# Performance work log

Hardware: AMD Instinct MI355X
Metric: run time of the kernel (lower is better)

## Reference

```python
import jax, jax.numpy as jnp
import numpy as np

BN_EPS = 1e-5


def setup_inputs() -> dict:
    key = jax.random.key(0)
    ks = jax.random.split(key, 6)
    B, N, M, C1, C2 = 8, 8192, 2048, 128, 256
    in_ch = C1 + C2  # 384
    return {
        "xyz1": jax.random.uniform(ks[0], (B, N, 3), dtype=jnp.float32),
        "xyz2": jax.random.uniform(ks[1], (B, M, 3), dtype=jnp.float32),
        "features1": jax.random.normal(ks[2], (B, C1, N), dtype=jnp.float32),
        "features2": jax.random.normal(ks[3], (B, C2, M), dtype=jnp.float32),
        # Conv1d(kernel_size=1, bias=False) weights, squeezed to [out, in]
        "conv_w0": jax.random.normal(ks[4], (256, in_ch), dtype=jnp.float32) * 0.05,
        "gamma0": jnp.ones((256,), dtype=jnp.float32),
        "beta0": jnp.zeros((256,), dtype=jnp.float32),
        "conv_w1": jax.random.normal(ks[5], (256, 256), dtype=jnp.float32) * 0.05,
        "gamma1": jnp.ones((256,), dtype=jnp.float32),
        "beta1": jnp.zeros((256,), dtype=jnp.float32),
    }


def _conv_bn_relu(x, w, gamma, beta):
    # 1x1 Conv1d (no bias) == per-point channel matmul: [B,Cin,N] -> [B,Cout,N]
    x = jnp.einsum("oc,bcn->bon", w, x)
    # BatchNorm1d in training mode: batch stats over (B, N), biased variance
    mu = jnp.mean(x, axis=(0, 2), keepdims=True)
    var = jnp.var(x, axis=(0, 2), keepdims=True)
    x = (x - mu) * jax.lax.rsqrt(var + BN_EPS)
    x = x * gamma[None, :, None] + beta[None, :, None]
    return jax.nn.relu(x)


def reference(xyz1, xyz2, features1, features2,
              conv_w0, gamma0, beta0, conv_w1, gamma1, beta1):
    # squared pairwise distances [B, N, M] (broadcast diff reduced over coord dim)
    diff = xyz1[:, :, None, :] - xyz2[:, None, :, :]  # [B,N,M,3]
    dists = jnp.sum(diff * diff, axis=-1)             # [B,N,M]
    idx = jnp.argmin(dists, axis=-1)                  # [B,N] nearest downsampled point

    # per-batch gather: features2[b, :, idx[b]] -> [B, C2, N]
    interp = jax.vmap(lambda f, i: f[:, i])(features2, idx)

    x = jnp.concatenate([features1, interp], axis=1)  # [B, C1+C2, N]
    x = _conv_bn_relu(x, conv_w0, gamma0, beta0)
    x = _conv_bn_relu(x, conv_w1, gamma1, beta1)
    return x
```

## Files before the change

kernel.cpp:

```cpp
#include <hip/hip_runtime.h>
#include <stdint.h>

typedef unsigned short u16;
typedef unsigned int u32;
typedef __attribute__((ext_vector_type(8))) short short8;
typedef __attribute__((ext_vector_type(4))) float floatx4;

__device__ __forceinline__ u16 f2b(float f) {
  union { float f; u32 u; } c; c.f = f;
  u32 u = c.u;
  u += 0x7fffu + ((u >> 16) & 1u);
  return (u16)(u >> 16);
}
__device__ __forceinline__ float b2f(u16 h) {
  union { u32 u; float f; } c; c.u = ((u32)h) << 16;
  return c.f;
}

__device__ __forceinline__ void glds16(const void* g, void* l) {
  __builtin_amdgcn_global_load_lds((__attribute__((address_space(1))) void*)g,
                                   (__attribute__((address_space(3))) void*)l, 16, 0, 0);
}

__global__ void prep_all_k(const float* __restrict__ xyz1, const float* __restrict__ xyz2,
                           float2* __restrict__ cand,
                           const float* __restrict__ f1, u16* __restrict__ f1t,
                           const float* __restrict__ f2, u16* __restrict__ f2t,
                           const float* __restrict__ w0, u16* __restrict__ w0b,
                           const float* __restrict__ w1, u16* __restrict__ w1b,
                           float* __restrict__ sums) {
  __shared__ __align__(16) char smem[9216];
  int blk = blockIdx.x, t = threadIdx.x;
  if (blk < 512) {
    float4* s2 = (float4*)smem;
    int nq = blk & 7, mq = (blk >> 3) & 7, b = blk >> 6;
    const float* x2 = xyz2 + ((size_t)b * 2048 + mq * 256) * 3;
    s2[t] = make_float4(x2[t * 3], x2[t * 3 + 1], x2[t * 3 + 2], 0.f);
    __syncthreads();
    int n0 = nq * 1024 + t;
    float px[4], py[4], pz[4];
#pragma unroll
    for (int q = 0; q < 4; q++) {
      const float* p1 = xyz1 + ((size_t)b * 8192 + n0 + q * 256) * 3;
      px[q] = p1[0]; py[q] = p1[1]; pz[q] = p1[2];
    }
    float best[4] = {3.0e38f, 3.0e38f, 3.0e38f, 3.0e38f};
    int bi[4] = {0, 0, 0, 0};
#pragma unroll 4
    for (int m = 0; m < 256; m++) {
      float4 qq = s2[m];
#pragma unroll
      for (int q = 0; q < 4; q++) {
        float dx = px[q] - qq.x, dy = py[q] - qq.y, dz = pz[q] - qq.z;
        float d = fmaf(dz, dz, fmaf(dy, dy, dx * dx));
        bool c = d < best[q];
        best[q] = c ? d : best[q];
        bi[q] = c ? m : bi[q];
      }
    }
#pragma unroll
    for (int q = 0; q < 4; q++) {
      int n = n0 + q * 256;
      cand[(size_t)mq * 65536 + (size_t)b * 8192 + n] =
          make_float2(best[q], __int_as_float(mq * 256 + bi[q]));
    }
  } else if (blk < 3584) {
    const float* in; u16* out; int C, N, bx, by, bz;
    if (blk < 2560) { int rel = blk - 512;  in = f1; out = f1t; C = 128; N = 8192; bx = rel & 127; by = (rel >> 7) & 1; bz = rel >> 8; }
    else            { int rel = blk - 2560; in = f2; out = f2t; C = 256; N = 2048; bx = rel & 31;  by = (rel >> 5) & 3; bz = rel >> 7; }
    u16 (*tile)[72] = (u16(*)[72])smem;
    int c0 = by * 64, n0 = bx * 64;
    const float* src = in + ((size_t)bz * C + c0) * N + n0;
#pragma unroll
    for (int i = 0; i < 4; i++) {
      int id = t + i * 256;
      int c = id >> 4, nq = (id & 15) * 4;
      float4 v = *(const float4*)(src + (size_t)c * N + nq);
      tile[nq + 0][c] = f2b(v.x);
      tile[nq + 1][c] = f2b(v.y);
      tile[nq + 2][c] = f2b(v.z);
      tile[nq + 3][c] = f2b(v.w);
    }
    __syncthreads();
    int n = t >> 2, ch = (t & 3) * 16;
    u16* dst = out + ((size_t)bz * N + n0 + n) * C + c0 + ch;
    *(uint4*)dst = *(const uint4*)&tile[n][ch];
    *(uint4*)(dst + 8) = *(const uint4*)&tile[n][ch + 8];
  } else {
    int rel = blk - 3584;
    int i = rel * 256 + t;
    if (rel < 384) w0b[i] = f2b(w0[i]);
    else { int j = i - 98304; w1b[j] = f2b(w1[j]); }
    if (rel < 4) sums[i] = 0.f;
  }
}

__global__ __launch_bounds__(512, 2) void gemm1_k(const u16* __restrict__ w0b, const u16* __restrict__ f1t,
                                                  const u16* __restrict__ f2t, const float2* __restrict__ cand,
                                                  float* __restrict__ sum0, float* __restrict__ sq0,
                                                  u16* __restrict__ y0) {
  __shared__ u16 Aw[128 * 384];
  int t = threadIdx.x;
  int bid = blockIdx.x;
  int ohalf = (bid >> 3) & 1;
  int pairidx = (bid & 7) | ((bid >> 4) << 3);
  int o0 = ohalf * 128;
  int lane = t & 63, wave = t >> 6;
  int wrow = (wave >> 2) * 64;
  int wp = (wave & 3) * 32;
  int lr = lane & 15, lq = lane >> 4;

#pragma unroll
  for (int it = 0; it < 12; it++) {
    u32 off = (u32)it * 8192 + (u32)t * 16;
    int row = off / 768;
    int c16 = (off - row * 768) >> 4;
    glds16(w0b + (size_t)(o0 + row) * 384 + ((c16 ^ (row & 7)) << 3),
           (char*)Aw + (size_t)it * 8192 + (size_t)wave * 1024);
  }

  float sa[4][4], qa[4][4];
#pragma unroll
  for (int i = 0; i < 4; i++)
#pragma unroll
    for (int r = 0; r < 4; r++) { sa[i][r] = 0.f; qa[i][r] = 0.f; }

  __syncthreads();

  for (int s = 0; s < 4; s++) {
    int pt0 = (pairidx * 4 + s) * 128;
    int b = pt0 >> 13;
    int gidx[2];
#pragma unroll
    for (int j = 0; j < 2; j++) {
      int p = pt0 + wp + j * 16 + lr;
      float bd = 3.0e38f; int bi = 0;
#pragma unroll
      for (int qc = 0; qc < 8; qc++) {
        float2 c = cand[(size_t)qc * 65536 + p];
        if (c.x < bd) { bd = c.x; bi = __float_as_int(c.y); }
      }
      gidx[j] = bi;
    }
    floatx4 zero = {0.f, 0.f, 0.f, 0.f};
    floatx4 acc[4][2];
#pragma unroll
    for (int i = 0; i < 4; i++)
#pragma unroll
      for (int j = 0; j < 2; j++) acc[i][j] = zero;

#pragma unroll
    for (int step = 0; step < 6; step++) {
      short8 bf[2][2];
#pragma unroll
      for (int ks = 0; ks < 2; ks++) {
#pragma unroll
        for (int j = 0; j < 2; j++) {
          int kk = ks * 32 + lq * 8;
          if (step < 2) {
            int p = pt0 + wp + j * 16 + lr;
            bf[ks][j] = *(const short8*)(f1t + (size_t)p * 128 + step * 64 + kk);
          } else {
            bf[ks][j] = *(const short8*)(f2t + ((size_t)(b << 11) + gidx[j]) * 256 +
                                         (step * 64 - 128) + kk);
          }
        }
      }
#pragma unroll
      for (int ks = 0; ks < 2; ks++) {
        short8 af[4];
#pragma unroll
        for (int i = 0; i < 4; i++) {
          int row = wrow + i * 16 + lr;
          af[i] = *(const short8*)&Aw[row * 384 + (((step * 8 + (ks << 2) + lq) ^ (lr & 7)) << 3)];
        }
#pragma unroll
        for (int i = 0; i < 4; i++)
#pragma unroll
          for (int j = 0; j < 2; j++)
            acc[i][j] = __builtin_amdgcn_mfma_f32_16x16x32_bf16(af[i], bf[ks][j], acc[i][j], 0, 0, 0);
      }
    }

#pragma unroll
    for (int i = 0; i < 4; i++) {
#pragma unroll
      for (int j = 0; j < 2; j++) {
        int o = o0 + wrow + i * 16 + lq * 4;
        int p = pt0 + wp + j * 16 + lr;
        uint2 pk;
        pk.x = (u32)f2b(acc[i][j][0]) | ((u32)f2b(acc[i][j][1]) << 16);
        pk.y = (u32)f2b(acc[i][j][2]) | ((u32)f2b(acc[i][j][3]) << 16);
        *(uint2*)&y0[(size_t)p * 256 + o] = pk;
      }
#pragma unroll
      for (int r = 0; r < 4; r++) {
        float v0 = acc[i][0][r], v1 = acc[i][1][r];
        sa[i][r] += v0 + v1;
        qa[i][r] += v0 * v0 + v1 * v1;
      }
    }
  }

#pragma unroll
  for (int i = 0; i < 4; i++)
#pragma unroll
    for (int r = 0; r < 4; r++)
#pragma unroll
      for (int m = 8; m >= 1; m >>= 1) {
        sa[i][r] += __shfl_xor(sa[i][r], m);
        qa[i][r] += __shfl_xor(qa[i][r], m);
      }
  __syncthreads();
  float* red = (float*)Aw;
  if (t < 256) red[t] = 0.f;
  __syncthreads();
  if (lr == 0) {
#pragma unroll
    for (int i = 0; i < 4; i++)
#pragma unroll
      for (int r = 0; r < 4; r++) {
        int o = wrow + i * 16 + lq * 4 + r;
        atomicAdd(&red[o], sa[i][r]);
        atomicAdd(&red[128 + o], qa[i][r]);
      }
  }
  __syncthreads();
  if (t < 128) {
    atomicAdd(&sum0[o0 + t], red[t]);
    atomicAdd(&sq0[o0 + t], red[128 + t]);
  }
}

__global__ __launch_bounds__(512, 2) void gemm2_k(const u16* __restrict__ w1b, const u16* __restrict__ y0,
                                                  const float* __restrict__ sum0, const float* __restrict__ sq0,
                                                  const float* __restrict__ gamma0, const float* __restrict__ beta0,
                                                  float* __restrict__ sum1, float* __restrict__ sq1,
                                                  u16* __restrict__ y1) {
  __shared__ u16 Aw[128 * 256];
  __shared__ u16 Bs[2][256 * 64];
  __shared__ float ssc[256], ssh[256];
  int t = threadIdx.x;
  int bid = blockIdx.x;
  int ohalf = (bid >> 3) & 1;
  int pairidx = (bid & 7) | ((bid >> 4) << 3);
  int o0 = ohalf * 128;
  int lane = t & 63, wave = t >> 6;
  int wrow = (wave >> 2) * 64;
  int wp = (wave & 3) * 64;
  int lr = lane & 15, lq = lane >> 4;
  if (t < 256) {
    float mean = sum0[t] * (1.f / 65536.f);
    float var = fmaxf(sq0[t] * (1.f / 65536.f) - mean * mean, 0.f);
    float r = rsqrtf(var + 1e-5f);
    float sc = gamma0[t] * r;
    ssc[t] = sc;
    ssh[t] = beta0[t] - mean * sc;
  }
#pragma unroll
  for (int it = 0; it < 8; it++) {
    u32 off = (u32)it * 8192 + (u32)t * 16;
    int row = off >> 9;
    int c16 = (off & 511) >> 4;
    glds16(w1b + (size_t)(o0 + row) * 256 + ((c16 ^ (row & 7)) << 3),
           (char*)Aw + (size_t)it * 8192 + (size_t)wave * 1024);
  }

  int brow[4], bpc[4], bch[4];
#pragma unroll
  for (int i = 0; i < 4; i++) {
    int id = t + i * 512;
    brow[i] = id >> 3; bpc[i] = id & 7;
    bch[i] = (bpc[i] ^ (brow[i] & 7)) * 8;
  }
  float sa[4][4], qa[4][4];
#pragma unroll
  for (int i = 0; i < 4; i++)
#pragma unroll
    for (int r = 0; r < 4; r++) { sa[i][r] = 0.f; qa[i][r] = 0.f; }

  __syncthreads();

  for (int s = 0; s < 2; s++) {
    int pt0 = (pairidx * 2 + s) * 256;
    uint4 rg[4];
    auto loadB = [&](int k0) {
#pragma unroll
      for (int i = 0; i < 4; i++)
        rg[i] = *(const uint4*)(y0 + (size_t)(pt0 + brow[i]) * 256 + k0 + bch[i]);
    };
    auto xformB = [&](int k0, int bufi) {
#pragma unroll
      for (int i = 0; i < 4; i++) {
        u32 rw[4] = {rg[i].x, rg[i].y, rg[i].z, rg[i].w};
        u32 ow[4];
#pragma unroll
        for (int w = 0; w < 4; w++) {
          int k = k0 + bch[i] + w * 2;
          float v0 = b2f((u16)(rw[w] & 0xffffu));
          float v1 = b2f((u16)(rw[w] >> 16));
          v0 = fmaxf(v0 * ssc[k] + ssh[k], 0.f);
          v1 = fmaxf(v1 * ssc[k + 1] + ssh[k + 1], 0.f);
          ow[w] = (u32)f2b(v0) | ((u32)f2b(v1) << 16);
        }
        uint4 ov; ov.x = ow[0]; ov.y = ow[1]; ov.z = ow[2]; ov.w = ow[3];
        *(uint4*)&Bs[bufi][brow[i] * 64 + bpc[i] * 8] = ov;
      }
    };
    floatx4 zero = {0.f, 0.f, 0.f, 0.f};
    floatx4 acc[4][4];
#pragma unroll
    for (int i = 0; i < 4; i++)
#pragma unroll
      for (int j = 0; j < 4; j++) acc[i][j] = zero;
    auto compute = [&](int k0, int bufi) {
#pragma unroll
      for (int ks = 0; ks < 2; ks++) {
        short8 af[4], bf[4];
#pragma unroll
        for (int i = 0; i < 4; i++) {
          int row = wrow + i * 16 + lr;
          af[i] = *(const short8*)&Aw[row * 256 + ((((k0 >> 3) + (ks << 2) + lq) ^ (lr & 7)) << 3)];
        }
#pragma unroll
        for (int j = 0; j < 4; j++) {
          int row = wp + j * 16 + lr;
          bf[j] = *(const short8*)&Bs[bufi][row * 64 + ((((ks << 2) | lq) ^ (lr & 7)) << 3)];
        }
#pragma unroll
        for (int i = 0; i < 4; i++)
#pragma unroll
          for (int j = 0; j < 4; j++)
            acc[i][j] = __builtin_amdgcn_mfma_f32_16x16x32_bf16(af[i], bf[j], acc[i][j], 0, 0, 0);
      }
    };

    loadB(0);
    xformB(0, 0);
    __syncthreads();
#pragma unroll
    for (int k0i = 0; k0i < 4; k0i++) {
      if (k0i < 3) loadB((k0i + 1) * 64);
      compute(k0i * 64, k0i & 1);
      __syncthreads();
      if (k0i < 3) {
        xformB((k0i + 1) * 64, (k0i + 1) & 1);
        __syncthreads();
      }
    }
#pragma unroll
    for (int i = 0; i < 4; i++) {
#pragma unroll
      for (int j = 0; j < 4; j++) {
        int o = o0 + wrow + i * 16 + lq * 4;
        int p = pt0 + wp + j * 16 + lr;
        uint2 pk;
        pk.x = (u32)f2b(acc[i][j][0]) | ((u32)f2b(acc[i][j][1]) << 16);
        pk.y = (u32)f2b(acc[i][j][2]) | ((u32)f2b(acc[i][j][3]) << 16);
        *(uint2*)&y1[(size_t)p * 256 + o] = pk;
      }
#pragma unroll
      for (int r = 0; r < 4; r++) {
        float v0 = acc[i][0][r], v1 = acc[i][1][r], v2 = acc[i][2][r], v3 = acc[i][3][r];
        sa[i][r] += v0 + v1 + v2 + v3;
        qa[i][r] += v0 * v0 + v1 * v1 + v2 * v2 + v3 * v3;
      }
    }
  }

#pragma unroll
  for (int i = 0; i < 4; i++)
#pragma unroll
    for (int r = 0; r < 4; r++)
#pragma unroll
      for (int m = 8; m >= 1; m >>= 1) {
        sa[i][r] += __shfl_xor(sa[i][r], m);
        qa[i][r] += __shfl_xor(qa[i][r], m);
      }
  __syncthreads();
  float* red = (float*)&Bs[0][0];
  if (t < 256) red[t] = 0.f;
  __syncthreads();
  if (lr == 0) {
#pragma unroll
    for (int i = 0; i < 4; i++)
#pragma unroll
      for (int r = 0; r < 4; r++) {
        int o = wrow + i * 16 + lq * 4 + r;
        atomicAdd(&red[o], sa[i][r]);
        atomicAdd(&red[128 + o], qa[i][r]);
      }
  }
  __syncthreads();
  if (t < 128) {
    atomicAdd(&sum1[o0 + t], red[t]);
    atomicAdd(&sq1[o0 + t], red[128 + t]);
  }
}

__global__ void finalize_k(const u16* __restrict__ y1, const float* __restrict__ sum1,
                           const float* __restrict__ sq1, const float* __restrict__ gamma1,
                           const float* __restrict__ beta1, float* __restrict__ out) {
  __shared__ float tile[64][65];
  __shared__ float fs[64], fh[64];
  int b = blockIdx.z, o0 = blockIdx.y * 64, n0 = blockIdx.x * 64;
  int t = threadIdx.x;
  if (t < 64) {
    int o = o0 + t;
    float mean = sum1[o] * (1.f / 65536.f);
    float var = fmaxf(sq1[o] * (1.f / 65536.f) - mean * mean, 0.f);
    float r = rsqrtf(var + 1e-5f);
    float sc = gamma1[o] * r;
    fs[t] = sc;
    fh[t] = beta1[o] - mean * sc;
  }
  __syncthreads();
  int pl = t >> 2, ch = (t & 3) * 16;
  const u16* src = y1 + ((size_t)(b * 8192 + n0 + pl)) * 256 + o0 + ch;
  uint4 r0 = *(const uint4*)src;
  uint4 r1 = *(const uint4*)(src + 8);
  u16 hv[16];
  *(uint4*)&hv[0] = r0;
  *(uint4*)&hv[8] = r1;
#pragma unroll
  for (int e = 0; e < 16; e++) {
    float v = b2f(hv[e]) * fs[ch + e] + fh[ch + e];
    tile[pl][ch + e] = fmaxf(v, 0.f);
  }
  __syncthreads();
  int ol = t >> 2, nch = (t & 3) * 16;
  float* dst = out + ((size_t)(b * 256 + o0 + ol)) * 8192 + n0 + nch;
#pragma unroll
  for (int j = 0; j < 16; j += 4) {
    float4 v = make_float4(tile[nch + j][ol], tile[nch + j + 1][ol],
                           tile[nch + j + 2][ol], tile[nch + j + 3][ol]);
    *(float4*)(dst + j) = v;
  }
}

extern "C" void kernel_launch(void* const* d_in, const int* in_sizes, int n_in,
                              void* d_out, int out_size, void* d_ws, size_t ws_size,
                              hipStream_t stream) {
  const float* xyz1      = (const float*)d_in[0];
  const float* xyz2      = (const float*)d_in[1];
  const float* features1 = (const float*)d_in[2];
  const float* features2 = (const float*)d_in[3];
  const float* conv_w0   = (const float*)d_in[4];
  const float* gamma0    = (const float*)d_in[5];
  const float* beta0     = (const float*)d_in[6];
  const float* conv_w1   = (const float*)d_in[7];
  const float* gamma1    = (const float*)d_in[8];
  const float* beta1     = (const float*)d_in[9];
  float* out = (float*)d_out;

  char* ws = (char*)d_ws;
  size_t off = 0;
  auto alloc = [&](size_t bytes) {
    char* p = ws + off;
    off = (off + bytes + 4095) & ~(size_t)4095;
    return p;
  };
  float*  sums = (float*)alloc(4 * 256 * 4);
  u16*    w0b  = (u16*)alloc(256 * 384 * 2);
  u16*    w1b  = (u16*)alloc(256 * 256 * 2);
  float2* cand = (float2*)alloc((size_t)8 * 65536 * 8);
  u16*    f1t  = (u16*)alloc((size_t)65536 * 128 * 2);
  u16*    f2t  = (u16*)alloc((size_t)16384 * 256 * 2);
  u16*    y0   = (u16*)alloc((size_t)65536 * 256 * 2);
  u16*    y1   = (u16*)alloc((size_t)65536 * 256 * 2);

  prep_all_k<<<dim3(4224), 256, 0, stream>>>(xyz1, xyz2, cand, features1, f1t,
                                             features2, f2t, conv_w0, w0b, conv_w1, w1b, sums);
  gemm1_k<<<dim3(256), 512, 0, stream>>>(w0b, f1t, f2t, cand, sums + 0, sums + 256, y0);
  gemm2_k<<<dim3(256), 512, 0, stream>>>(w1b, y0, sums + 0, sums + 256, gamma0, beta0,
                                         sums + 512, sums + 768, y1);
  finalize_k<<<dim3(128, 4, 8), 256, 0, stream>>>(y1, sums + 512, sums + 768, gamma1, beta1, out);
}
```

Before: 270.7 us.

## Keep conv0 weights in registers and double-buffer B tiles via LDS in gemm1

gemm1 now runs 512 blocks of 256 threads instead of 256 blocks of 512. Each wave holds its 64x384 slice of the bf16 weights in registers (48 short8 per lane) instead of staging the whole weight tile in LDS. Point features, both direct and gathered, are staged into a small swizzled double buffer in LDS with global_load_lds, so the load for the next K step overlaps the MFMAs on the current one. The BN statistics are reduced per tile straight into a shared array. The large register footprint may force spills or lower occupancy, and a barrier is added on every K step.

Result: faster. 247.1 us (-8.7%).

```diff
diff --git a/kernel.cpp b/kernel.cpp
--- a/kernel.cpp
+++ b/kernel.cpp
@@ -95,52 +95,49 @@
   }
 }
 
-__global__ __launch_bounds__(512, 2) void gemm1_k(const u16* __restrict__ w0b, const u16* __restrict__ f1t,
+__global__ __launch_bounds__(256, 2) void gemm1_k(const u16* __restrict__ w0b, const u16* __restrict__ f1t,
                                                   const u16* __restrict__ f2t, const float2* __restrict__ cand,
                                                   float* __restrict__ sum0, float* __restrict__ sq0,
                                                   u16* __restrict__ y0) {
-  __shared__ u16 Aw[128 * 384];
+  __shared__ u16 Bs[2][64 * 64];
+  __shared__ float red[256];
   int t = threadIdx.x;
   int bid = blockIdx.x;
   int ohalf = (bid >> 3) & 1;
   int pairidx = (bid & 7) | ((bid >> 4) << 3);
   int o0 = ohalf * 128;
   int lane = t & 63, wave = t >> 6;
-  int wrow = (wave >> 2) * 64;
-  int wp = (wave & 3) * 32;
+  int wrow = (wave >> 1) * 64;
+  int wp = (wave & 1) * 32;
   int lr = lane & 15, lq = lane >> 4;
-
-#pragma unroll
-  for (int it = 0; it < 12; it++) {
-    u32 off = (u32)it * 8192 + (u32)t * 16;
-    int row = off / 768;
-    int c16 = (off - row * 768) >> 4;
-    glds16(w0b + (size_t)(o0 + row) * 384 + ((c16 ^ (row & 7)) << 3),
-           (char*)Aw + (size_t)it * 8192 + (size_t)wave * 1024);
-  }
-
-  float sa[4][4], qa[4][4];
-#pragma unroll
-  for (int i = 0; i < 4; i++)
-#pragma unroll
-    for (int r = 0; r < 4; r++) { sa[i][r] = 0.f; qa[i][r] = 0.f; }
-
-  __syncthreads();
+  int srow = lane >> 3;
+  int sch = ((lane & 7) ^ srow) * 8;
+
+  red[t] = 0.f;
+
+  short8 areg[4][12];
+#pragma unroll
+  for (int i = 0; i < 4; i++) {
+    const u16* wr = w0b + (size_t)(o0 + wrow + i * 16 + lr) * 384 + lq * 8;
+#pragma unroll
+    for (int kf = 0; kf < 12; kf++)
+      areg[i][kf] = *(const short8*)(wr + kf * 32);
+  }
 
   for (int s = 0; s < 4; s++) {
-    int pt0 = (pairidx * 4 + s) * 128;
-    int b = pt0 >> 13;
+    int pt0 = (pairidx * 4 + s) * 64;
+    size_t bb = (size_t)((pt0 >> 13) << 11);
     int gidx[2];
 #pragma unroll
-    for (int j = 0; j < 2; j++) {
-      int p = pt0 + wp + j * 16 + lr;
+    for (int i = 0; i < 2; i++) {
+      int p = pt0 + (wave * 2 + i) * 8 + srow;
       float bd = 3.0e38f; int bi = 0;
 #pragma unroll
       for (int qc = 0; qc < 8; qc++) {
         float2 c = cand[(size_t)qc * 65536 + p];
         if (c.x < bd) { bd = c.x; bi = __float_as_int(c.y); }
       }
-      gidx[j] = bi;
+      gidx[i] = bi;
     }
     floatx4 zero = {0.f, 0.f, 0.f, 0.f};
     floatx4 acc[4][2];
@@ -149,37 +146,37 @@
 #pragma unroll
       for (int j = 0; j < 2; j++) acc[i][j] = zero;
 
+    auto stageB = [&](int step, int bufi) {
+#pragma unroll
+      for (int i = 0; i < 2; i++) {
+        int row = (wave * 2 + i) * 8 + srow;
+        const u16* src;
+        if (step < 2) src = f1t + (size_t)(pt0 + row) * 128 + step * 64 + sch;
+        else          src = f2t + (bb + gidx[i]) * 256 + (step * 64 - 128) + sch;
+        glds16(src, &Bs[bufi][(wave * 2 + i) * 512]);
+      }
+    };
+
+    stageB(0, 0);
+    __syncthreads();
 #pragma unroll
     for (int step = 0; step < 6; step++) {
-      short8 bf[2][2];
+      if (step < 5) stageB(step + 1, (step + 1) & 1);
 #pragma unroll
       for (int ks = 0; ks < 2; ks++) {
-#pragma unroll
-        for (int j = 0; j < 2; j++) {
-          int kk = ks * 32 + lq * 8;
-          if (step < 2) {
-            int p = pt0 + wp + j * 16 + lr;
-            bf[ks][j] = *(const short8*)(f1t + (size_t)p * 128 + step * 64 + kk);
-          } else {
-            bf[ks][j] = *(const short8*)(f2t + ((size_t)(b << 11) + gidx[j]) * 256 +
-                                         (step * 64 - 128) + kk);
-          }
-        }
-      }
-#pragma unroll
-      for (int ks = 0; ks < 2; ks++) {
-        short8 af[4];
-#pragma unroll
-        for (int i = 0; i < 4; i++) {
-          int row = wrow + i * 16 + lr;
-          af[i] = *(const short8*)&Aw[row * 384 + (((step * 8 + (ks << 2) + lq) ^ (lr & 7)) << 3)];
-        }
+        short8 bf[2];
+#pragma unroll
+        for (int j = 0; j < 2; j++)
+          bf[j] = *(const short8*)&Bs[step & 1][(wp + j * 16 + lr) * 64 +
+                                               ((((ks << 2) | lq) ^ (lr & 7)) << 3)];
+        int kf = step * 2 + ks;
 #pragma unroll
         for (int i = 0; i < 4; i++)
 #pragma unroll
           for (int j = 0; j < 2; j++)
-            acc[i][j] = __builtin_amdgcn_mfma_f32_16x16x32_bf16(af[i], bf[ks][j], acc[i][j], 0, 0, 0);
-      }
+            acc[i][j] = __builtin_amdgcn_mfma_f32_16x16x32_bf16(areg[i][kf], bf[j], acc[i][j], 0, 0, 0);
+      }
+      __syncthreads();
     }
 
 #pragma unroll
@@ -195,36 +192,19 @@
       }
 #pragma unroll
       for (int r = 0; r < 4; r++) {
-        float v0 = acc[i][0][r], v1 = acc[i][1][r];
-        sa[i][r] += v0 + v1;
-        qa[i][r] += v0 * v0 + v1 * v1;
-      }
-    }
-  }
-
-#pragma unroll
-  for (int i = 0; i < 4; i++)
-#pragma unroll
-    for (int r = 0; r < 4; r++)
-#pragma unroll
-      for (int m = 8; m >= 1; m >>= 1) {
-        sa[i][r] += __shfl_xor(sa[i][r], m);
-        qa[i][r] += __shfl_xor(qa[i][r], m);
-      }
-  __syncthreads();
-  float* red = (float*)Aw;
-  if (t < 256) red[t] = 0.f;
-  __syncthreads();
-  if (lr == 0) {
-#pragma unroll
-    for (int i = 0; i < 4; i++)
-#pragma unroll
-      for (int r = 0; r < 4; r++) {
-        int o = wrow + i * 16 + lq * 4 + r;
-        atomicAdd(&red[o], sa[i][r]);
-        atomicAdd(&red[128 + o], qa[i][r]);
-      }
-  }
+        float sv = acc[i][0][r] + acc[i][1][r];
+        float qv = acc[i][0][r] * acc[i][0][r] + acc[i][1][r] * acc[i][1][r];
+#pragma unroll
+        for (int m = 8; m >= 1; m >>= 1) { sv += __shfl_xor(sv, m); qv += __shfl_xor(qv, m); }
+        if (lr == 0) {
+          int o = wrow + i * 16 + lq * 4 + r;
+          atomicAdd(&red[o], sv);
+          atomicAdd(&red[128 + o], qv);
+        }
+      }
+    }
+  }
+
   __syncthreads();
   if (t < 128) {
     atomicAdd(&sum0[o0 + t], red[t]);
@@ -471,7 +451,7 @@
 
   prep_all_k<<<dim3(4224), 256, 0, stream>>>(xyz1, xyz2, cand, features1, f1t,
                                              features2, f2t, conv_w0, w0b, conv_w1, w1b, sums);
-  gemm1_k<<<dim3(256), 512, 0, stream>>>(w0b, f1t, f2t, cand, sums + 0, sums + 256, y0);
+  gemm1_k<<<dim3(512), 256, 0, stream>>>(w0b, f1t, f2t, cand, sums + 0, sums + 256, y0);
   gemm2_k<<<dim3(256), 512, 0, stream>>>(w1b, y0, sums + 0, sums + 256, gamma0, beta0,
                                          sums + 512, sums + 768, y1);
   finalize_k<<<dim3(128, 4, 8), 256, 0, stream>>>(y1, sums + 512, sums + 768, gamma1, beta1, out);
```
